# Optimization experiments

Hardware: AMD Instinct MI355X
Metric: run time of the kernel (lower is better)

## Reference

```python
import jax, jax.numpy as jnp
import numpy as np

B, S, D = 8, 2048, 128

def setup_inputs() -> dict:
    key = jax.random.key(0)
    kq, kk, kv = jax.random.split(key, 3)
    return {
        "query": jax.random.normal(kq, (B, S, D), dtype=jnp.float32),
        "key": jax.random.normal(kk, (B, S, D), dtype=jnp.float32),
        "value": jax.random.normal(kv, (B, S, D), dtype=jnp.float32),
    }

def reference(query, key, value):
    # softmax(QK^T / sqrt(d_k)) V, no mask, dropout=0
    d_k = query.shape[-1]
    scale = 1.0 / np.sqrt(d_k).astype(np.float32)
    # [B, Sq, Sk]
    attn_scores = jnp.einsum('bqd,bkd->bqk', query, key) * scale
    attn_weights = jax.nn.softmax(attn_scores, axis=-1)
    # [B, Sq, Dv]
    output = jnp.einsum('bqk,bkd->bqd', attn_weights, value)
    return (output, attn_weights)
```

## Files before the change

kernel.cpp:

```cpp
#include <hip/hip_runtime.h>
#include <hip/hip_bf16.h>

#define NB 8
#define SS 2048
#define DD 128
#define NQK (NB * SS * DD)

typedef __attribute__((ext_vector_type(8))) short bf16x8;
typedef __attribute__((ext_vector_type(16))) float f32x16;
typedef __attribute__((ext_vector_type(4))) float f32x4;
typedef __attribute__((ext_vector_type(4))) unsigned int uint4v;
typedef __attribute__((ext_vector_type(2))) unsigned int uint2v;

static constexpr float C1 = 0.08838834764831845f * 1.4426950408889634f;

#define MFMA32(a, b, c) __builtin_amdgcn_mfma_f32_32x32x16_bf16(a, b, c, 0, 0, 0)
#define PSWAP(a, b) __builtin_amdgcn_permlane32_swap(a, b, false, false)

#if __has_builtin(__builtin_amdgcn_exp2f)
#define EXP2 __builtin_amdgcn_exp2f
#else
#define EXP2 exp2f
#endif

__device__ __forceinline__ unsigned short f2bf(float x) {
  __hip_bfloat16 h = __float2bfloat16(x);
  unsigned short r;
  __builtin_memcpy(&r, &h, 2);
  return r;
}

__device__ __forceinline__ void nt_store4(const float* src, float* dst) {
  f32x4 v;
  __builtin_memcpy(&v, src, 16);
  __builtin_nontemporal_store(v, (f32x4*)dst);
}

__global__ __launch_bounds__(256)
void prep_kernel(const float* __restrict__ Q, const float* __restrict__ K,
                 const float* __restrict__ V, unsigned short* __restrict__ Qt,
                 unsigned short* __restrict__ Kt, unsigned short* __restrict__ Vt) {
  __shared__ __align__(16) float Tf[32][132];
  const int ti = blockIdx.x, b = blockIdx.y, role = blockIdx.z;
  const int tid = threadIdx.x;
  const float* src = role == 0 ? Q : (role == 1 ? K : V);
  {
    const int row = tid >> 3, seg = (tid & 7) * 16;
    const float4* sp = (const float4*)(src + ((size_t)b * SS + ti * 32 + row) * DD + seg);
#pragma unroll
    for (int j = 0; j < 4; ++j) *(float4*)&Tf[row][seg + 4 * j] = sp[j];
  }
  __syncthreads();
  if (role < 2) {
    unsigned short* dst = (role == 0 ? Qt : Kt) + ((size_t)b * 64 + ti) * 4096;
#pragma unroll
    for (int e = 0; e < 2; ++e) {
      const int c = 2 * tid + e, lq = c & 31, ck = c >> 5;
      const float4 a = *(const float4*)&Tf[lq][ck * 8];
      const float4 d = *(const float4*)&Tf[lq][ck * 8 + 4];
      bf16x8 o;
      o[0] = (short)f2bf(a.x); o[1] = (short)f2bf(a.y);
      o[2] = (short)f2bf(a.z); o[3] = (short)f2bf(a.w);
      o[4] = (short)f2bf(d.x); o[5] = (short)f2bf(d.y);
      o[6] = (short)f2bf(d.z); o[7] = (short)f2bf(d.w);
      *(bf16x8*)(dst + c * 8) = o;
    }
  } else {
    unsigned short* dst = Vt + ((size_t)b * 64 + ti) * 4096;
#pragma unroll
    for (int e = 0; e < 2; ++e) {
      const int chunk = 2 * tid + e, cc = chunk >> 7, d = chunk & 127;
      bf16x8 o;
#pragma unroll
      for (int j = 0; j < 8; ++j) o[j] = (short)f2bf(Tf[cc * 8 + j][d]);
      *(bf16x8*)(dst + chunk * 8) = o;
    }
  }
}

__global__ __launch_bounds__(256, 2)
void attn_kernel(const unsigned short* __restrict__ Qt,
                 const unsigned short* __restrict__ Kt,
                 const unsigned short* __restrict__ Vt,
                 float* __restrict__ W, float* __restrict__ Out) {
  __shared__ __align__(16) float PW[4][32][40];
  __shared__ __align__(16) float R[32][132];
  __shared__ float2 sms[4][32];

  const int bid = blockIdx.x;
  const int b = bid & 7, qb = bid >> 3;
  const int q0 = qb * 32;
  const int tid = threadIdx.x;
  const int lane = tid & 63, wv = tid >> 6;
  const int lq = lane & 31, h2 = lane >> 5;
  const f32x16 ZERO16 = {0, 0, 0, 0, 0, 0, 0, 0, 0, 0, 0, 0, 0, 0, 0, 0};

  {
    float* Rf = &R[0][0];
    for (int idx = tid; idx < 32 * 132; idx += 256) Rf[idx] = 0.f;
  }

  const unsigned short* qbase = Qt + ((size_t)b * 64 + (q0 >> 5)) * 4096;
  bf16x8 qh[8];
#pragma unroll
  for (int ds = 0; ds < 8; ++ds)
    qh[ds] = *(const bf16x8*)(qbase + ((ds * 2 + h2) * 32 + lq) * 8);

  const unsigned short* const Ktb = Kt + (size_t)b * 64 * 4096;
  const unsigned short* const Vtb = Vt + (size_t)b * 64 * 4096;

  float m2 = -1e30f, s2 = 0.f;
#pragma unroll
  for (int kp = 0; kp < 8; ++kp) {
    const unsigned short* kb0 = Ktb + (size_t)(wv * 16 + 2 * kp) * 4096;
    const unsigned short* kb1 = kb0 + 4096;
    bf16x8 a0[8], a1[8];
#pragma unroll
    for (int ds = 0; ds < 8; ++ds) {
      a0[ds] = *(const bf16x8*)(kb0 + ((ds * 2 + h2) * 32 + lq) * 8);
      a1[ds] = *(const bf16x8*)(kb1 + ((ds * 2 + h2) * 32 + lq) * 8);
    }
    f32x16 acc0 = ZERO16, acc1 = ZERO16;
#pragma unroll
    for (int ds = 0; ds < 8; ++ds) {
      acc0 = MFMA32(a0[ds], qh[ds], acc0);
      acc1 = MFMA32(a1[ds], qh[ds], acc1);
    }
    float tm0 = acc0[0], tm1 = acc1[0];
#pragma unroll
    for (int r = 1; r < 16; ++r) {
      tm0 = fmaxf(tm0, acc0[r]);
      tm1 = fmaxf(tm1, acc1[r]);
    }
    const float nm2 = fmaxf(m2, fmaxf(tm0, tm1) * C1);
    float add = 0.f;
#pragma unroll
    for (int r = 0; r < 16; ++r)
      add += EXP2(fmaf(acc0[r], C1, -nm2)) + EXP2(fmaf(acc1[r], C1, -nm2));
    s2 = s2 * EXP2(m2 - nm2) + add;
    m2 = nm2;
  }
  {
    const float mo = __shfl_xor(m2, 32);
    const float so = __shfl_xor(s2, 32);
    const float nm = fmaxf(m2, mo);
    s2 = s2 * EXP2(m2 - nm) + so * EXP2(mo - nm);
    if (h2 == 0) sms[wv][lq] = make_float2(nm, s2);
  }
  __syncthreads();
  float lb;
  {
    float2 pj[4];
    float m = -1e30f;
#pragma unroll
    for (int j = 0; j < 4; ++j) {
      pj[j] = sms[j][lq];
      m = fmaxf(m, pj[j].x);
    }
    float s = 0.f;
#pragma unroll
    for (int j = 0; j < 4; ++j) s += pj[j].y * EXP2(pj[j].x - m);
    lb = -(m + __log2f(s));
  }

  float* pwwr[4];
#pragma unroll
  for (int g = 0; g < 4; ++g)
    pwwr[g] = &PW[wv][lq][(8 * g + 4 * h2 + lq * 4) & 31];
  const int gq8 = lane >> 3, gks = lane & 7;
  const float* pwrd[4];
  float* wgb[4];
#pragma unroll
  for (int i = 0; i < 4; ++i) {
    const int row = i * 8 + gq8;
    pwrd[i] = &PW[wv][row][(gks * 4 + row * 4) & 31];
    wgb[i] = W + ((size_t)b * SS + q0 + row) * SS + gks * 4;
  }

  f32x16 accO[4];
#pragma unroll
  for (int dt = 0; dt < 4; ++dt) accO[dt] = ZERO16;

  f32x16 acc = ZERO16;
  bf16x8 vb[8];
  {
    const int t0 = 4 * (qb & 15) + wv;
    const unsigned short* k0 = Ktb + (size_t)t0 * 4096;
    const unsigned short* v0 = Vtb + (size_t)t0 * 4096;
    bf16x8 ah[8];
#pragma unroll
    for (int ds = 0; ds < 8; ++ds)
      ah[ds] = *(const bf16x8*)(k0 + ((ds * 2 + h2) * 32 + lq) * 8);
#pragma unroll
    for (int ds = 0; ds < 8; ++ds) acc = MFMA32(ah[ds], qh[ds], acc);
#pragma unroll
    for (int kk = 0; kk < 2; ++kk)
#pragma unroll
      for (int dt = 0; dt < 4; ++dt)
        vb[kk * 4 + dt] =
            *(const bf16x8*)(v0 + ((kk * 2 + h2) * 128 + dt * 32 + lq) * 8);
  }

  for (int kt = 0; kt < 16; ++kt) {
    const int tile = 4 * ((kt + qb) & 15) + wv;
    const int kb = tile * 32;
    bf16x8 ahn[8], vbn[8];
    if (kt < 15) {
      const int tn = 4 * ((kt + 1 + qb) & 15) + wv;
      const unsigned short* kn = Ktb + (size_t)tn * 4096;
      const unsigned short* vn = Vtb + (size_t)tn * 4096;
#pragma unroll
      for (int ds = 0; ds < 8; ++ds)
        ahn[ds] = *(const bf16x8*)(kn + ((ds * 2 + h2) * 32 + lq) * 8);
#pragma unroll
      for (int kk = 0; kk < 2; ++kk)
#pragma unroll
        for (int dt = 0; dt < 4; ++dt)
          vbn[kk * 4 + dt] =
              *(const bf16x8*)(vn + ((kk * 2 + h2) * 128 + dt * 32 + lq) * 8);
    }
    unsigned int U[8];
#pragma unroll
    for (int g = 0; g < 4; ++g) {
      const float p0 = EXP2(fmaf(acc[4 * g + 0], C1, lb));
      const float p1 = EXP2(fmaf(acc[4 * g + 1], C1, lb));
      const float p2 = EXP2(fmaf(acc[4 * g + 2], C1, lb));
      const float p3 = EXP2(fmaf(acc[4 * g + 3], C1, lb));
      *(float4*)pwwr[g] = make_float4(p0, p1, p2, p3);
      U[2 * g] = (unsigned)f2bf(p0) | ((unsigned)f2bf(p1) << 16);
      U[2 * g + 1] = (unsigned)f2bf(p2) | ((unsigned)f2bf(p3) << 16);
    }
    f32x16 accn = ZERO16;
    if (kt < 15) {
#pragma unroll
      for (int ds = 0; ds < 8; ++ds) accn = MFMA32(ahn[ds], qh[ds], accn);
    }
#pragma unroll
    for (int i = 0; i < 4; ++i) nt_store4(pwrd[i], wgb[i] + kb);
    const uint2v s02 = PSWAP(U[0], U[2]);
    const uint2v s13 = PSWAP(U[1], U[3]);
    const uint2v s46 = PSWAP(U[4], U[6]);
    const uint2v s57 = PSWAP(U[5], U[7]);
    uint4v w0, w1;
    w0.x = s02.x; w0.y = s13.x; w0.z = s02.y; w0.w = s13.y;
    w1.x = s46.x; w1.y = s57.x; w1.z = s46.y; w1.w = s57.y;
    const bf16x8 pa0 = __builtin_bit_cast(bf16x8, w0);
    const bf16x8 pa1 = __builtin_bit_cast(bf16x8, w1);
#pragma unroll
    for (int dt = 0; dt < 4; ++dt) accO[dt] = MFMA32(pa0, vb[dt], accO[dt]);
#pragma unroll
    for (int dt = 0; dt < 4; ++dt) accO[dt] = MFMA32(pa1, vb[4 + dt], accO[dt]);
    acc = accn;
#pragma unroll
    for (int j = 0; j < 8; ++j) vb[j] = vbn[j];
  }

  __syncthreads();
#pragma unroll
  for (int ph = 0; ph < 4; ++ph) {
    if (wv == ph) {
#pragma unroll
      for (int dt = 0; dt < 4; ++dt) {
#pragma unroll
        for (int r = 0; r < 16; ++r) {
          const int q = (r & 3) + 8 * (r >> 2) + 4 * h2;
          R[q][dt * 32 + lq] += accO[dt][r];
        }
      }
    }
    __syncthreads();
  }
  {
    const int row = tid >> 3, c0 = (tid & 7) * 16;
    float* ob = Out + ((size_t)b * SS + q0 + row) * DD + c0;
#pragma unroll
    for (int j = 0; j < 4; ++j) nt_store4(&R[row][c0 + 4 * j], ob + 4 * j);
  }
}

extern "C" void kernel_launch(void* const* d_in, const int* in_sizes, int n_in,
                              void* d_out, int out_size, void* d_ws, size_t ws_size,
                              hipStream_t stream) {
  const float* Q = (const float*)d_in[0];
  const float* K = (const float*)d_in[1];
  const float* V = (const float*)d_in[2];
  float* out = (float*)d_out;
  float* W = out + (size_t)NQK;

  char* ws = (char*)d_ws;
  unsigned short* Qt = (unsigned short*)(ws);
  unsigned short* Kt = (unsigned short*)(ws + ((size_t)4 << 20));
  unsigned short* Vt = (unsigned short*)(ws + ((size_t)8 << 20));

  prep_kernel<<<dim3(64, 8, 3), 256, 0, stream>>>(Q, K, V, Qt, Kt, Vt);
  attn_kernel<<<512, 256, 0, stream>>>(Qt, Kt, Vt, W, out);
}
```

Baseline: 63.81 us.

## Drop register prefetch pipeline to cut VGPRs and raise occupancy to three

Removes the software-pipelined prefetch of the next K/V tile and its lookahead QK MFMA, and splits the stats pass from two tiles per iteration to one, rolling that loop. It raises launch bounds to allow three blocks per CU and switches the W stores from nontemporal to normal stores. The aim is to lower register pressure so more waves can hide latency, at the cost of exposing load latency inside each wave.

```diff
diff --git a/kernel.cpp b/kernel.cpp
--- a/kernel.cpp
+++ b/kernel.cpp
@@ -28,6 +28,12 @@
   unsigned short r;
   __builtin_memcpy(&r, &h, 2);
   return r;
+}
+
+__device__ __forceinline__ void st4(const float* src, float* dst) {
+  f32x4 v;
+  __builtin_memcpy(&v, src, 16);
+  *(f32x4*)dst = v;
 }
 
 __device__ __forceinline__ void nt_store4(const float* src, float* dst) {
@@ -78,7 +84,7 @@
   }
 }
 
-__global__ __launch_bounds__(256, 2)
+__global__ __launch_bounds__(256, 3)
 void attn_kernel(const unsigned short* __restrict__ Qt,
                  const unsigned short* __restrict__ Kt,
                  const unsigned short* __restrict__ Vt,
@@ -110,33 +116,22 @@
   const unsigned short* const Vtb = Vt + (size_t)b * 64 * 4096;
 
   float m2 = -1e30f, s2 = 0.f;
-#pragma unroll
-  for (int kp = 0; kp < 8; ++kp) {
-    const unsigned short* kb0 = Ktb + (size_t)(wv * 16 + 2 * kp) * 4096;
-    const unsigned short* kb1 = kb0 + 4096;
-    bf16x8 a0[8], a1[8];
-#pragma unroll
-    for (int ds = 0; ds < 8; ++ds) {
+  for (int kp = 0; kp < 16; ++kp) {
+    const unsigned short* kb0 = Ktb + (size_t)(wv * 16 + kp) * 4096;
+    bf16x8 a0[8];
+#pragma unroll
+    for (int ds = 0; ds < 8; ++ds)
       a0[ds] = *(const bf16x8*)(kb0 + ((ds * 2 + h2) * 32 + lq) * 8);
-      a1[ds] = *(const bf16x8*)(kb1 + ((ds * 2 + h2) * 32 + lq) * 8);
-    }
-    f32x16 acc0 = ZERO16, acc1 = ZERO16;
-#pragma unroll
-    for (int ds = 0; ds < 8; ++ds) {
-      acc0 = MFMA32(a0[ds], qh[ds], acc0);
-      acc1 = MFMA32(a1[ds], qh[ds], acc1);
-    }
-    float tm0 = acc0[0], tm1 = acc1[0];
-#pragma unroll
-    for (int r = 1; r < 16; ++r) {
-      tm0 = fmaxf(tm0, acc0[r]);
-      tm1 = fmaxf(tm1, acc1[r]);
-    }
-    const float nm2 = fmaxf(m2, fmaxf(tm0, tm1) * C1);
+    f32x16 acc0 = ZERO16;
+#pragma unroll
+    for (int ds = 0; ds < 8; ++ds) acc0 = MFMA32(a0[ds], qh[ds], acc0);
+    float tm0 = acc0[0];
+#pragma unroll
+    for (int r = 1; r < 16; ++r) tm0 = fmaxf(tm0, acc0[r]);
+    const float nm2 = fmaxf(m2, tm0 * C1);
     float add = 0.f;
 #pragma unroll
-    for (int r = 0; r < 16; ++r)
-      add += EXP2(fmaf(acc0[r], C1, -nm2)) + EXP2(fmaf(acc1[r], C1, -nm2));
+    for (int r = 0; r < 16; ++r) add += EXP2(fmaf(acc0[r], C1, -nm2));
     s2 = s2 * EXP2(m2 - nm2) + add;
     m2 = nm2;
   }
@@ -181,44 +176,18 @@
 #pragma unroll
   for (int dt = 0; dt < 4; ++dt) accO[dt] = ZERO16;
 
-  f32x16 acc = ZERO16;
-  bf16x8 vb[8];
-  {
-    const int t0 = 4 * (qb & 15) + wv;
-    const unsigned short* k0 = Ktb + (size_t)t0 * 4096;
-    const unsigned short* v0 = Vtb + (size_t)t0 * 4096;
-    bf16x8 ah[8];
-#pragma unroll
-    for (int ds = 0; ds < 8; ++ds)
-      ah[ds] = *(const bf16x8*)(k0 + ((ds * 2 + h2) * 32 + lq) * 8);
-#pragma unroll
-    for (int ds = 0; ds < 8; ++ds) acc = MFMA32(ah[ds], qh[ds], acc);
-#pragma unroll
-    for (int kk = 0; kk < 2; ++kk)
-#pragma unroll
-      for (int dt = 0; dt < 4; ++dt)
-        vb[kk * 4 + dt] =
-            *(const bf16x8*)(v0 + ((kk * 2 + h2) * 128 + dt * 32 + lq) * 8);
-  }
-
   for (int kt = 0; kt < 16; ++kt) {
     const int tile = 4 * ((kt + qb) & 15) + wv;
     const int kb = tile * 32;
-    bf16x8 ahn[8], vbn[8];
-    if (kt < 15) {
-      const int tn = 4 * ((kt + 1 + qb) & 15) + wv;
-      const unsigned short* kn = Ktb + (size_t)tn * 4096;
-      const unsigned short* vn = Vtb + (size_t)tn * 4096;
-#pragma unroll
-      for (int ds = 0; ds < 8; ++ds)
-        ahn[ds] = *(const bf16x8*)(kn + ((ds * 2 + h2) * 32 + lq) * 8);
-#pragma unroll
-      for (int kk = 0; kk < 2; ++kk)
-#pragma unroll
-        for (int dt = 0; dt < 4; ++dt)
-          vbn[kk * 4 + dt] =
-              *(const bf16x8*)(vn + ((kk * 2 + h2) * 128 + dt * 32 + lq) * 8);
-    }
+    const unsigned short* ktile = Ktb + (size_t)tile * 4096;
+    const unsigned short* vtile = Vtb + (size_t)tile * 4096;
+    bf16x8 ah[8];
+#pragma unroll
+    for (int ds = 0; ds < 8; ++ds)
+      ah[ds] = *(const bf16x8*)(ktile + ((ds * 2 + h2) * 32 + lq) * 8);
+    f32x16 acc = ZERO16;
+#pragma unroll
+    for (int ds = 0; ds < 8; ++ds) acc = MFMA32(ah[ds], qh[ds], acc);
     unsigned int U[8];
 #pragma unroll
     for (int g = 0; g < 4; ++g) {
@@ -230,13 +199,6 @@
       U[2 * g] = (unsigned)f2bf(p0) | ((unsigned)f2bf(p1) << 16);
       U[2 * g + 1] = (unsigned)f2bf(p2) | ((unsigned)f2bf(p3) << 16);
     }
-    f32x16 accn = ZERO16;
-    if (kt < 15) {
-#pragma unroll
-      for (int ds = 0; ds < 8; ++ds) accn = MFMA32(ahn[ds], qh[ds], accn);
-    }
-#pragma unroll
-    for (int i = 0; i < 4; ++i) nt_store4(pwrd[i], wgb[i] + kb);
     const uint2v s02 = PSWAP(U[0], U[2]);
     const uint2v s13 = PSWAP(U[1], U[3]);
     const uint2v s46 = PSWAP(U[4], U[6]);
@@ -247,12 +209,18 @@
     const bf16x8 pa0 = __builtin_bit_cast(bf16x8, w0);
     const bf16x8 pa1 = __builtin_bit_cast(bf16x8, w1);
 #pragma unroll
-    for (int dt = 0; dt < 4; ++dt) accO[dt] = MFMA32(pa0, vb[dt], accO[dt]);
-#pragma unroll
-    for (int dt = 0; dt < 4; ++dt) accO[dt] = MFMA32(pa1, vb[4 + dt], accO[dt]);
-    acc = accn;
-#pragma unroll
-    for (int j = 0; j < 8; ++j) vb[j] = vbn[j];
+    for (int i = 0; i < 4; ++i) st4(pwrd[i], wgb[i] + kb);
+#pragma unroll
+    for (int dt = 0; dt < 4; ++dt) {
+      const bf16x8 vb0 = *(const bf16x8*)(vtile + ((h2)*128 + dt * 32 + lq) * 8);
+      accO[dt] = MFMA32(pa0, vb0, accO[dt]);
+    }
+#pragma unroll
+    for (int dt = 0; dt < 4; ++dt) {
+      const bf16x8 vb1 =
+          *(const bf16x8*)(vtile + ((2 + h2) * 128 + dt * 32 + lq) * 8);
+      accO[dt] = MFMA32(pa1, vb1, accO[dt]);
+    }
   }
 
   __syncthreads();
```

New measurement: 71.96 us. +12.8%, slower.

## Prefetch K tiles two iterations ahead and use regular stores for weights

Applied to the files above, without the earlier changes.

K fragments are now loaded two iterations ahead, through a second register buffer, instead of one. The next QK^T MFMA chain is moved after the PV MFMAs so it sits later in the loop. The attention-weight writes to global memory switch from nontemporal to ordinary vector stores. The intent is to hide more global-load latency and reorder MFMA work. In exchange it uses more VGPRs, which may lower occupancy, and it changes cache behaviour for the large weight output.

```diff
diff --git a/kernel.cpp b/kernel.cpp
--- a/kernel.cpp
+++ b/kernel.cpp
@@ -28,6 +28,12 @@
   unsigned short r;
   __builtin_memcpy(&r, &h, 2);
   return r;
+}
+
+__device__ __forceinline__ void st4(const float* src, float* dst) {
+  f32x4 v;
+  __builtin_memcpy(&v, src, 16);
+  *(f32x4*)dst = v;
 }
 
 __device__ __forceinline__ void nt_store4(const float* src, float* dst) {
@@ -182,11 +188,13 @@
   for (int dt = 0; dt < 4; ++dt) accO[dt] = ZERO16;
 
   f32x16 acc = ZERO16;
-  bf16x8 vb[8];
+  bf16x8 vb[8], ahB[8];
   {
     const int t0 = 4 * (qb & 15) + wv;
+    const int t1 = 4 * ((1 + qb) & 15) + wv;
     const unsigned short* k0 = Ktb + (size_t)t0 * 4096;
     const unsigned short* v0 = Vtb + (size_t)t0 * 4096;
+    const unsigned short* k1 = Ktb + (size_t)t1 * 4096;
     bf16x8 ah[8];
 #pragma unroll
     for (int ds = 0; ds < 8; ++ds)
@@ -199,19 +207,25 @@
       for (int dt = 0; dt < 4; ++dt)
         vb[kk * 4 + dt] =
             *(const bf16x8*)(v0 + ((kk * 2 + h2) * 128 + dt * 32 + lq) * 8);
+#pragma unroll
+    for (int ds = 0; ds < 8; ++ds)
+      ahB[ds] = *(const bf16x8*)(k1 + ((ds * 2 + h2) * 32 + lq) * 8);
   }
 
   for (int kt = 0; kt < 16; ++kt) {
     const int tile = 4 * ((kt + qb) & 15) + wv;
     const int kb = tile * 32;
-    bf16x8 ahn[8], vbn[8];
+    bf16x8 ahA[8], vbn[8];
+    if (kt < 14) {
+      const int tn2 = 4 * ((kt + 2 + qb) & 15) + wv;
+      const unsigned short* kn = Ktb + (size_t)tn2 * 4096;
+#pragma unroll
+      for (int ds = 0; ds < 8; ++ds)
+        ahA[ds] = *(const bf16x8*)(kn + ((ds * 2 + h2) * 32 + lq) * 8);
+    }
     if (kt < 15) {
       const int tn = 4 * ((kt + 1 + qb) & 15) + wv;
-      const unsigned short* kn = Ktb + (size_t)tn * 4096;
       const unsigned short* vn = Vtb + (size_t)tn * 4096;
-#pragma unroll
-      for (int ds = 0; ds < 8; ++ds)
-        ahn[ds] = *(const bf16x8*)(kn + ((ds * 2 + h2) * 32 + lq) * 8);
 #pragma unroll
       for (int kk = 0; kk < 2; ++kk)
 #pragma unroll
@@ -230,13 +244,8 @@
       U[2 * g] = (unsigned)f2bf(p0) | ((unsigned)f2bf(p1) << 16);
       U[2 * g + 1] = (unsigned)f2bf(p2) | ((unsigned)f2bf(p3) << 16);
     }
-    f32x16 accn = ZERO16;
-    if (kt < 15) {
-#pragma unroll
-      for (int ds = 0; ds < 8; ++ds) accn = MFMA32(ahn[ds], qh[ds], accn);
-    }
-#pragma unroll
-    for (int i = 0; i < 4; ++i) nt_store4(pwrd[i], wgb[i] + kb);
+#pragma unroll
+    for (int i = 0; i < 4; ++i) st4(pwrd[i], wgb[i] + kb);
     const uint2v s02 = PSWAP(U[0], U[2]);
     const uint2v s13 = PSWAP(U[1], U[3]);
     const uint2v s46 = PSWAP(U[4], U[6]);
@@ -250,9 +259,16 @@
     for (int dt = 0; dt < 4; ++dt) accO[dt] = MFMA32(pa0, vb[dt], accO[dt]);
 #pragma unroll
     for (int dt = 0; dt < 4; ++dt) accO[dt] = MFMA32(pa1, vb[4 + dt], accO[dt]);
-    acc = accn;
+    if (kt < 15) {
+      f32x16 a2 = ZERO16;
+#pragma unroll
+      for (int ds = 0; ds < 8; ++ds) a2 = MFMA32(ahB[ds], qh[ds], a2);
+      acc = a2;
+    }
 #pragma unroll
     for (int j = 0; j < 8; ++j) vb[j] = vbn[j];
+#pragma unroll
+    for (int j = 0; j < 8; ++j) ahB[j] = ahA[j];
   }
 
   __syncthreads();
```

Result: no change. 63.20 us (-1.0%).
